# Kernel tuning notes

Measured on AMD Instinct MI355X. Metric: run time of the kernel, lower is better.

Reference implementation:

```python
import jax, jax.numpy as jnp
import numpy as np

NUM_HEADS = 8
WINDOW = 7      # window_size -> K = 49 neighbors
DILATION = 1


def setup_inputs() -> dict:
    key = jax.random.key(0)
    k1, k2, k3 = jax.random.split(key, 3)
    shape = (4, 256, 48, 48)  # [B, C, H, W], C = num_heads * d_head
    return {
        "q": jax.random.normal(k1, shape, jnp.float32),
        "k": jax.random.normal(k2, shape, jnp.float32),
        "v": jax.random.normal(k3, shape, jnp.float32),
    }


def _neighbors(x, window, dilation):
    # x: [B, h, d, H, W] -> [B, h, K, d, H, W] via pad-and-slice shifts
    B, h, d, H, W = x.shape
    r = window // 2
    p = r * dilation
    xp = jnp.pad(x, ((0, 0), (0, 0), (0, 0), (p, p), (p, p)))
    offs = [(i - r) * dilation for i in range(window)]
    sl = [xp[:, :, :, p + dy:p + dy + H, p + dx:p + dx + W]
          for dy in offs for dx in offs]
    return jnp.stack(sl, axis=2)


def _valid_mask(H, W, window, dilation):
    # [K, H, W] boolean: True where the shifted neighbor is in-bounds
    r = window // 2
    offs = np.array([(i - r) * dilation for i in range(window)])
    hy = np.arange(H)[None, :] + offs[:, None]  # [window, H]
    wx = np.arange(W)[None, :] + offs[:, None]  # [window, W]
    vh = (hy >= 0) & (hy < H)
    vw = (wx >= 0) & (wx < W)
    mask = vh[:, None, :, None] & vw[None, :, None, :]  # [window, window, H, W]
    return jnp.asarray(mask.reshape(window * window, H, W))


def reference(q, k, v):
    B, C, H, W = q.shape
    h = NUM_HEADS
    d = C // h
    qh = q.reshape(B, h, d, H, W)
    kh = k.reshape(B, h, d, H, W)
    vh = v.reshape(B, h, d, H, W)
    kn = _neighbors(kh, WINDOW, DILATION)  # [B,h,K,d,H,W]
    vn = _neighbors(vh, WINDOW, DILATION)
    mask = _valid_mask(H, W, WINDOW, DILATION)[None, None]  # [1,1,K,H,W]
    scores = jnp.einsum('bhdxy,bhkdxy->bhkxy', qh, kn) * (d ** -0.5)
    scores = jnp.where(mask, scores, jnp.finfo(scores.dtype).min)
    attn = jax.nn.softmax(scores, axis=2)
    out = jnp.einsum('bhkxy,bhkdxy->bhdxy', attn, vn)
    return out.reshape(B, C, H, W)  # merge_heads
```

## Files before the change

### kernel.cpp

```cpp
#include <hip/hip_runtime.h>


#define H_IMG 48
#define W_IMG 48
#define DHEAD 32
#define NH    8
#define RAD   3
#define TW    16
#define TH    6
#define NPART 4
#define CPL   8
#define HALO_W  (TW + 2*RAD)
#define HALO_H  (TH + 2*RAD)
#define HALO_PX (HALO_W * HALO_H)
#define CSTR    40
#define PLANE   (H_IMG * W_IMG)
#define NTHREADS (NPART * TW * TH)

typedef _Float16 half_t;
typedef half_t half2_t __attribute__((ext_vector_type(2)));

__device__ __forceinline__ float dppadd1(float x) {
  int y = __builtin_amdgcn_update_dpp(0, __float_as_int(x), 0xB1, 0xF, 0xF, true);
  return x + __int_as_float(y);
}
__device__ __forceinline__ float dppadd2(float x) {
  int y = __builtin_amdgcn_update_dpp(0, __float_as_int(x), 0x4E, 0xF, 0xF, true);
  return x + __int_as_float(y);
}

__global__ __launch_bounds__(NTHREADS, 4)
void natten_f32_kernel(const float* __restrict__ q,
                       const float* __restrict__ k,
                       const float* __restrict__ v,
                       float* __restrict__ out) {
  __shared__ __align__(16) unsigned short kl[(HALO_PX + 1) * CSTR];
  __shared__ __align__(16) unsigned short vl[(HALO_PX + 1) * CSTR];

  const int part = threadIdx.x;
  const int qx   = threadIdx.y;
  const int qy   = threadIdx.z;
  const int tid  = part + NPART * qx + NPART * TW * qy;
  const int x0   = blockIdx.x * TW;
  const int y0   = blockIdx.y * TH;
  const size_t cbase = (size_t)blockIdx.z * DHEAD * PLANE;

  for (int i = tid; i < HALO_PX * 2 * (DHEAD / 2); i += NTHREADS) {
    const int p    = i % HALO_PX;
    const int rest = i / HALO_PX;
    const int j    = rest & 15;
    const float* __restrict__ src = (rest & 16) ? v : k;
    unsigned short* dst           = (rest & 16) ? vl : kl;
    const int hy = p / HALO_W;
    const int hx = p - hy * HALO_W;
    const int gy = y0 - RAD + hy;
    const int gx = x0 - RAD + hx;
    union { half2_t h; unsigned int u; } pk;
    pk.u = 0;
    if ((unsigned)gy < (unsigned)H_IMG && (unsigned)gx < (unsigned)W_IMG) {
      const size_t g = cbase + (size_t)(2 * j) * PLANE + (size_t)gy * W_IMG + gx;
      pk.h.x = (half_t)src[g];
      pk.h.y = (half_t)src[g + PLANE];
    }
    *(unsigned int*)&dst[p * CSTR + 2 * j] = pk.u;
  }
  if (tid < CSTR) {
    kl[HALO_PX * CSTR + tid] = 0;
    vl[HALO_PX * CSTR + tid] = 0;
  }

  const int gqx = x0 + qx, gqy = y0 + qy;
  const float S = 0.17677669529663687f;
  const size_t qoff = cbase + (size_t)gqy * W_IMG + gqx;
  half2_t qp[4];
#pragma unroll
  for (int j = 0; j < 4; ++j) {
    qp[j].x = (half_t)(q[qoff + (size_t)(part * CPL + 2 * j) * PLANE] * S);
    qp[j].y = (half_t)(q[qoff + (size_t)(part * CPL + 2 * j + 1) * PLANE] * S);
  }

  unsigned colmask = 0;
#pragma unroll
  for (int rx = 0; rx < 7; ++rx) {
    const int gx = gqx + rx - RAD;
    if ((unsigned)gx < (unsigned)W_IMG) colmask |= (1u << rx);
  }

  __syncthreads();

  float den = 0.0f;
  float o[CPL];
#pragma unroll
  for (int j = 0; j < CPL; ++j) o[j] = 0.0f;

  for (int ry = 0; ry < 2 * RAD + 1; ++ry) {
    const int gy = gqy + ry - RAD;
    const unsigned mrow = ((unsigned)gy < (unsigned)H_IMG) ? colmask : 0u;
    const int base = ((qy + ry) * HALO_W + qx) * CSTR + part * CPL;
    const unsigned short* kb = &kl[base];
    const unsigned short* vb = &vl[base];
#pragma unroll
    for (int rx = 0; rx < 8; ++rx) {
      union { uint4 u; half2_t h[4]; } kw, vw;
      kw.u = *(const uint4*)(kb + rx * CSTR);
      vw.u = *(const uint4*)(vb + rx * CSTR);
      float acc = __builtin_amdgcn_fdot2(qp[0], kw.h[0], 0.0f, false);
      acc = __builtin_amdgcn_fdot2(qp[1], kw.h[1], acc, false);
      acc = __builtin_amdgcn_fdot2(qp[2], kw.h[2], acc, false);
      acc = __builtin_amdgcn_fdot2(qp[3], kw.h[3], acc, false);
      acc = dppadd1(acc);
      acc = dppadd2(acc);
      const float pe = __expf(acc);
      const float p = (mrow & (1u << rx)) ? pe : 0.0f;
      den += p;
      o[0] += p * (float)vw.h[0].x;  o[1] += p * (float)vw.h[0].y;
      o[2] += p * (float)vw.h[1].x;  o[3] += p * (float)vw.h[1].y;
      o[4] += p * (float)vw.h[2].x;  o[5] += p * (float)vw.h[2].y;
      o[6] += p * (float)vw.h[3].x;  o[7] += p * (float)vw.h[3].y;
    }
  }

  const float rden = 1.0f / den;
#pragma unroll
  for (int j = 0; j < CPL; ++j)
    out[qoff + (size_t)(part * CPL + j) * PLANE] = o[j] * rden;
}

extern "C" void kernel_launch(void* const* d_in, const int* in_sizes, int n_in,
                              void* d_out, int out_size, void* d_ws, size_t ws_size,
                              hipStream_t stream) {
  const float* q = (const float*)d_in[0];
  const float* k = (const float*)d_in[1];
  const float* v = (const float*)d_in[2];
  float* out = (float*)d_out;

  dim3 grid(W_IMG / TW, H_IMG / TH, 4 * NH);
  dim3 block(NPART, TW, TH);
  hipLaunchKernelGGL(natten_f32_kernel, grid, block, 0, stream, q, k, v, out);
}
```

Before: 110.1 us.

## Compute neighborhood QK and PV with MFMA over a 32-wide band per row

Replaces the per-thread fdot2 dot products with 16x16x32 f16 MFMA instructions. Each wave handles one query row of 16 pixels and computes scores against a 32-pixel band of keys per window row, masking out-of-window entries. The exponentiated probabilities go through a per-wave LDS buffer and are then multiplied by V with another MFMA. K and V are staged in new LDS layouts (V transposed to channel-major) so they fit the MFMA operands. The cost is computing scores for 32 band columns instead of the 7 window columns, plus the extra LDS round trip for the probabilities.

```diff
diff --git a/kernel.cpp b/kernel.cpp
--- a/kernel.cpp
+++ b/kernel.cpp
@@ -5,125 +5,147 @@
 #define W_IMG 48
 #define DHEAD 32
 #define NH    8
-#define RAD   3
+#define PLANE (H_IMG * W_IMG)
 #define TW    16
 #define TH    6
-#define NPART 4
-#define CPL   8
-#define HALO_W  (TW + 2*RAD)
-#define HALO_H  (TH + 2*RAD)
-#define HALO_PX (HALO_W * HALO_H)
-#define CSTR    40
-#define PLANE   (H_IMG * W_IMG)
-#define NTHREADS (NPART * TW * TH)
+#define KROWS 12
+#define KSTR  36
+#define VSTR  392
+#define PSTR  36
 
 typedef _Float16 half_t;
 typedef half_t half2_t __attribute__((ext_vector_type(2)));
+typedef half_t half8_t __attribute__((ext_vector_type(8)));
+typedef float  f32x4   __attribute__((ext_vector_type(4)));
 
-__device__ __forceinline__ float dppadd1(float x) {
-  int y = __builtin_amdgcn_update_dpp(0, __float_as_int(x), 0xB1, 0xF, 0xF, true);
-  return x + __int_as_float(y);
-}
-__device__ __forceinline__ float dppadd2(float x) {
-  int y = __builtin_amdgcn_update_dpp(0, __float_as_int(x), 0x4E, 0xF, 0xF, true);
-  return x + __int_as_float(y);
-}
+__global__ __launch_bounds__(64 * TH, 2)
+void natten_mfma_kernel(const float* __restrict__ q,
+                        const float* __restrict__ k,
+                        const float* __restrict__ v,
+                        float* __restrict__ out) {
+  __shared__ __align__(16) unsigned short kl[KROWS * 32 * KSTR];
+  __shared__ __align__(16) unsigned short vl[DHEAD * VSTR];
+  __shared__ __align__(16) unsigned short Pbuf[TH * TW * PSTR];
 
-__global__ __launch_bounds__(NTHREADS, 4)
-void natten_f32_kernel(const float* __restrict__ q,
-                       const float* __restrict__ k,
-                       const float* __restrict__ v,
-                       float* __restrict__ out) {
-  __shared__ __align__(16) unsigned short kl[(HALO_PX + 1) * CSTR];
-  __shared__ __align__(16) unsigned short vl[(HALO_PX + 1) * CSTR];
-
-  const int part = threadIdx.x;
-  const int qx   = threadIdx.y;
-  const int qy   = threadIdx.z;
-  const int tid  = part + NPART * qx + NPART * TW * qy;
+  const int lane = threadIdx.x;
+  const int wy   = threadIdx.y;
+  const int tid  = wy * 64 + lane;
   const int x0   = blockIdx.x * TW;
   const int y0   = blockIdx.y * TH;
   const size_t cbase = (size_t)blockIdx.z * DHEAD * PLANE;
 
-  for (int i = tid; i < HALO_PX * 2 * (DHEAD / 2); i += NTHREADS) {
-    const int p    = i % HALO_PX;
-    const int rest = i / HALO_PX;
-    const int j    = rest & 15;
-    const float* __restrict__ src = (rest & 16) ? v : k;
-    unsigned short* dst           = (rest & 16) ? vl : kl;
-    const int hy = p / HALO_W;
-    const int hx = p - hy * HALO_W;
-    const int gy = y0 - RAD + hy;
-    const int gx = x0 - RAD + hx;
-    union { half2_t h; unsigned int u; } pk;
-    pk.u = 0;
+  for (int i = tid; i < 16 * KROWS * 32; i += 64 * TH) {
+    const int px = i & 31;
+    const int t  = i >> 5;
+    const int hr = t % KROWS;
+    const int c  = t / KROWS;
+    const int gy = y0 - 3 + hr, gx = x0 - 3 + px;
+    union { half2_t h; unsigned u; } pk; pk.u = 0;
     if ((unsigned)gy < (unsigned)H_IMG && (unsigned)gx < (unsigned)W_IMG) {
-      const size_t g = cbase + (size_t)(2 * j) * PLANE + (size_t)gy * W_IMG + gx;
-      pk.h.x = (half_t)src[g];
-      pk.h.y = (half_t)src[g + PLANE];
+      const float* kb = k + cbase + (size_t)(2 * c) * PLANE + gy * W_IMG + gx;
+      pk.h.x = (half_t)kb[0];
+      pk.h.y = (half_t)kb[PLANE];
     }
-    *(unsigned int*)&dst[p * CSTR + 2 * j] = pk.u;
+    *(unsigned*)&kl[(hr * 32 + px) * KSTR + 2 * c] = pk.u;
   }
-  if (tid < CSTR) {
-    kl[HALO_PX * CSTR + tid] = 0;
-    vl[HALO_PX * CSTR + tid] = 0;
+  for (int i = tid; i < DHEAD * KROWS * 16; i += 64 * TH) {
+    const int xp = i & 15;
+    const int t  = i >> 4;
+    const int hr = t % KROWS;
+    const int ch = t / KROWS;
+    const int gy = y0 - 3 + hr;
+    const int gx0 = x0 - 3 + 2 * xp;
+    union { half2_t h; unsigned u; } pv; pv.u = 0;
+    if ((unsigned)gy < (unsigned)H_IMG) {
+      const float* vb = v + cbase + (size_t)ch * PLANE + gy * W_IMG;
+      if ((unsigned)gx0 < (unsigned)W_IMG)       pv.h.x = (half_t)vb[gx0];
+      if ((unsigned)(gx0 + 1) < (unsigned)W_IMG) pv.h.y = (half_t)vb[gx0 + 1];
+    }
+    *(unsigned*)&vl[ch * VSTR + hr * 32 + 2 * xp] = pv.u;
   }
 
-  const int gqx = x0 + qx, gqy = y0 + qy;
+  const int qi = lane & 15;
+  const int Q  = lane >> 4;
+  const int gqy = y0 + wy;
   const float S = 0.17677669529663687f;
-  const size_t qoff = cbase + (size_t)gqy * W_IMG + gqx;
-  half2_t qp[4];
+  union { half8_t h; uint4 u; } qf;
+  {
+    const float* qb = q + cbase + (size_t)gqy * W_IMG + x0 + qi;
 #pragma unroll
-  for (int j = 0; j < 4; ++j) {
-    qp[j].x = (half_t)(q[qoff + (size_t)(part * CPL + 2 * j) * PLANE] * S);
-    qp[j].y = (half_t)(q[qoff + (size_t)(part * CPL + 2 * j + 1) * PLANE] * S);
+    for (int j = 0; j < 8; ++j)
+      qf.h[j] = (half_t)(qb[(size_t)(Q * 8 + j) * PLANE] * S);
   }
 
-  unsigned colmask = 0;
-#pragma unroll
-  for (int rx = 0; rx < 7; ++rx) {
-    const int gx = gqx + rx - RAD;
-    if ((unsigned)gx < (unsigned)W_IMG) colmask |= (1u << rx);
-  }
+  const int xq = x0 + qi;
+  const int lft = (xq < 3) ? xq : 3;
+  const int rgt = (47 - xq < 3) ? (47 - xq) : 3;
+  const unsigned pm = ((1u << (lft + rgt + 1)) - 1u) << (qi + 3 - lft);
 
   __syncthreads();
 
-  float den = 0.0f;
-  float o[CPL];
+  unsigned short* Pb = &Pbuf[wy * TW * PSTR];
+  f32x4 o0 = {0.f, 0.f, 0.f, 0.f};
+  f32x4 o1 = {0.f, 0.f, 0.f, 0.f};
+  float den_l = 0.f;
+
+  for (int d = 0; d < 7; ++d) {
+    const int hr = wy + d;
+    const int gy = gqy + d - 3;
+    const unsigned pmr = ((unsigned)gy < (unsigned)H_IMG) ? pm : 0u;
+
+    const unsigned short* krow = &kl[hr * 32 * KSTR];
+    union { uint4 u; half8_t h; } A0, A1;
+    {
+      const unsigned short* p0 = &krow[qi * KSTR + Q * 8];
+      const unsigned short* p1 = &krow[(qi + 16) * KSTR + Q * 8];
+      uint2 a = *(const uint2*)p0, b = *(const uint2*)(p0 + 4);
+      uint2 c = *(const uint2*)p1, e = *(const uint2*)(p1 + 4);
+      A0.u = make_uint4(a.x, a.y, b.x, b.y);
+      A1.u = make_uint4(c.x, c.y, e.x, e.y);
+    }
+    f32x4 zero = {0.f, 0.f, 0.f, 0.f};
+    f32x4 s0 = __builtin_amdgcn_mfma_f32_16x16x32_f16(A0.h, qf.h, zero, 0, 0, 0);
+    f32x4 s1 = __builtin_amdgcn_mfma_f32_16x16x32_f16(A1.h, qf.h, zero, 0, 0, 0);
+
+    union { half_t h[4]; uint2 u; } w0, w1;
 #pragma unroll
-  for (int j = 0; j < CPL; ++j) o[j] = 0.0f;
+    for (int r = 0; r < 4; ++r) {
+      const int p0i = 4 * Q + r;
+      const float e0 = (pmr >> p0i) & 1 ? __expf(s0[r]) : 0.f;
+      const float e1 = (pmr >> (p0i + 16)) & 1 ? __expf(s1[r]) : 0.f;
+      den_l += e0 + e1;
+      w0.h[r] = (half_t)e0;
+      w1.h[r] = (half_t)e1;
+    }
+    *(uint2*)&Pb[qi * PSTR + 4 * Q]      = w0.u;
+    *(uint2*)&Pb[qi * PSTR + 16 + 4 * Q] = w1.u;
+    __builtin_amdgcn_wave_barrier();
+    union { uint4 u; half8_t h; } Pf;
+    {
+      const unsigned short* pр = &Pb[qi * PSTR + 8 * Q];
+      uint2 a = *(const uint2*)pр, b = *(const uint2*)(pр + 4);
+      Pf.u = make_uint4(a.x, a.y, b.x, b.y);
+    }
+    __builtin_amdgcn_wave_barrier();
 
-  for (int ry = 0; ry < 2 * RAD + 1; ++ry) {
-    const int gy = gqy + ry - RAD;
-    const unsigned mrow = ((unsigned)gy < (unsigned)H_IMG) ? colmask : 0u;
-    const int base = ((qy + ry) * HALO_W + qx) * CSTR + part * CPL;
-    const unsigned short* kb = &kl[base];
-    const unsigned short* vb = &vl[base];
-#pragma unroll
-    for (int rx = 0; rx < 8; ++rx) {
-      union { uint4 u; half2_t h[4]; } kw, vw;
-      kw.u = *(const uint4*)(kb + rx * CSTR);
-      vw.u = *(const uint4*)(vb + rx * CSTR);
-      float acc = __builtin_amdgcn_fdot2(qp[0], kw.h[0], 0.0f, false);
-      acc = __builtin_amdgcn_fdot2(qp[1], kw.h[1], acc, false);
-      acc = __builtin_amdgcn_fdot2(qp[2], kw.h[2], acc, false);
-      acc = __builtin_amdgcn_fdot2(qp[3], kw.h[3], acc, false);
-      acc = dppadd1(acc);
-      acc = dppadd2(acc);
-      const float pe = __expf(acc);
-      const float p = (mrow & (1u << rx)) ? pe : 0.0f;
-      den += p;
-      o[0] += p * (float)vw.h[0].x;  o[1] += p * (float)vw.h[0].y;
-      o[2] += p * (float)vw.h[1].x;  o[3] += p * (float)vw.h[1].y;
-      o[4] += p * (float)vw.h[2].x;  o[5] += p * (float)vw.h[2].y;
-      o[6] += p * (float)vw.h[3].x;  o[7] += p * (float)vw.h[3].y;
-    }
+    union { uint4 u; half8_t h; } V0, V1;
+    V0.u = *(const uint4*)&vl[qi * VSTR + hr * 32 + 8 * Q];
+    V1.u = *(const uint4*)&vl[(qi + 16) * VSTR + hr * 32 + 8 * Q];
+
+    o0 = __builtin_amdgcn_mfma_f32_16x16x32_f16(V0.h, Pf.h, o0, 0, 0, 0);
+    o1 = __builtin_amdgcn_mfma_f32_16x16x32_f16(V1.h, Pf.h, o1, 0, 0, 0);
   }
 
-  const float rden = 1.0f / den;
+  den_l += __shfl_xor(den_l, 16, 64);
+  den_l += __shfl_xor(den_l, 32, 64);
+  const float rden = 1.0f / den_l;
+
+  float* ob = out + cbase + (size_t)gqy * W_IMG + x0 + qi;
 #pragma unroll
-  for (int j = 0; j < CPL; ++j)
-    out[qoff + (size_t)(part * CPL + j) * PLANE] = o[j] * rden;
+  for (int r = 0; r < 4; ++r) {
+    ob[(size_t)(4 * Q + r) * PLANE]      = o0[r] * rden;
+    ob[(size_t)(16 + 4 * Q + r) * PLANE] = o1[r] * rden;
+  }
 }
 
 extern "C" void kernel_launch(void* const* d_in, const int* in_sizes, int n_in,
@@ -135,6 +157,6 @@
   float* out = (float*)d_out;
 
   dim3 grid(W_IMG / TW, H_IMG / TH, 4 * NH);
-  dim3 block(NPART, TW, TH);
-  hipLaunchKernelGGL(natten_f32_kernel, grid, block, 0, stream, q, k, v, out);
+  dim3 block(64, TH);
+  hipLaunchKernelGGL(natten_mfma_kernel, grid, block, 0, stream, q, k, v, out);
 }
```

Result: slower. 124.3 us (+12.9%).

## Use two lanes per query, exp2 softmax, and packed fp16 PV accumulation

Applied to the files above, without the earlier changes.

Each query is now split across 2 lanes of 16 channels instead of 4 lanes of 8, and the tile grows to 16x8. This halves the DPP reductions and lets the halo be shared by more queries. Scores are pre-scaled by log2(e) and go through a native exp2, with masked neighbors set to a large negative value instead of being selected after exp. The output accumulates in packed half2 FMA instead of fp32. That cuts VALU work but risks precision loss, since unnormalized fp16 sums could lose accuracy or overflow.

```diff
diff --git a/kernel.cpp b/kernel.cpp
--- a/kernel.cpp
+++ b/kernel.cpp
@@ -7,15 +7,13 @@
 #define NH    8
 #define RAD   3
 #define TW    16
-#define TH    6
-#define NPART 4
-#define CPL   8
+#define TH    8
 #define HALO_W  (TW + 2*RAD)
 #define HALO_H  (TH + 2*RAD)
 #define HALO_PX (HALO_W * HALO_H)
-#define CSTR    40
+#define CSTR    36
 #define PLANE   (H_IMG * W_IMG)
-#define NTHREADS (NPART * TW * TH)
+#define NTHREADS 256
 
 typedef _Float16 half_t;
 typedef half_t half2_t __attribute__((ext_vector_type(2)));
@@ -24,12 +22,8 @@
   int y = __builtin_amdgcn_update_dpp(0, __float_as_int(x), 0xB1, 0xF, 0xF, true);
   return x + __int_as_float(y);
 }
-__device__ __forceinline__ float dppadd2(float x) {
-  int y = __builtin_amdgcn_update_dpp(0, __float_as_int(x), 0x4E, 0xF, 0xF, true);
-  return x + __int_as_float(y);
-}
 
-__global__ __launch_bounds__(NTHREADS, 4)
+__global__ __launch_bounds__(NTHREADS, 3)
 void natten_f32_kernel(const float* __restrict__ q,
                        const float* __restrict__ k,
                        const float* __restrict__ v,
@@ -40,29 +34,28 @@
   const int part = threadIdx.x;
   const int qx   = threadIdx.y;
   const int qy   = threadIdx.z;
-  const int tid  = part + NPART * qx + NPART * TW * qy;
+  const int tid  = part + 2 * qx + 32 * qy;
   const int x0   = blockIdx.x * TW;
   const int y0   = blockIdx.y * TH;
   const size_t cbase = (size_t)blockIdx.z * DHEAD * PLANE;
 
-  for (int i = tid; i < HALO_PX * 2 * (DHEAD / 2); i += NTHREADS) {
-    const int p    = i % HALO_PX;
+  for (int i = tid; i < HALO_PX * 32; i += NTHREADS) {
+    const int px   = i % HALO_PX;
     const int rest = i / HALO_PX;
     const int j    = rest & 15;
     const float* __restrict__ src = (rest & 16) ? v : k;
     unsigned short* dst           = (rest & 16) ? vl : kl;
-    const int hy = p / HALO_W;
-    const int hx = p - hy * HALO_W;
+    const int hy = px / HALO_W;
+    const int hx = px - hy * HALO_W;
     const int gy = y0 - RAD + hy;
     const int gx = x0 - RAD + hx;
-    union { half2_t h; unsigned int u; } pk;
-    pk.u = 0;
+    union { half2_t h; unsigned u; } pk; pk.u = 0;
     if ((unsigned)gy < (unsigned)H_IMG && (unsigned)gx < (unsigned)W_IMG) {
       const size_t g = cbase + (size_t)(2 * j) * PLANE + (size_t)gy * W_IMG + gx;
       pk.h.x = (half_t)src[g];
       pk.h.y = (half_t)src[g + PLANE];
     }
-    *(unsigned int*)&dst[p * CSTR + 2 * j] = pk.u;
+    *(unsigned*)&dst[px * CSTR + 2 * j] = pk.u;
   }
   if (tid < CSTR) {
     kl[HALO_PX * CSTR + tid] = 0;
@@ -70,13 +63,13 @@
   }
 
   const int gqx = x0 + qx, gqy = y0 + qy;
-  const float S = 0.17677669529663687f;
+  const float Sl = 0.17677669529663687f * 1.4426950408889634f;
   const size_t qoff = cbase + (size_t)gqy * W_IMG + gqx;
-  half2_t qp[4];
+  half2_t qp[8];
 #pragma unroll
-  for (int j = 0; j < 4; ++j) {
-    qp[j].x = (half_t)(q[qoff + (size_t)(part * CPL + 2 * j) * PLANE] * S);
-    qp[j].y = (half_t)(q[qoff + (size_t)(part * CPL + 2 * j + 1) * PLANE] * S);
+  for (int j = 0; j < 8; ++j) {
+    qp[j].x = (half_t)(q[qoff + (size_t)(part * 16 + 2 * j) * PLANE] * Sl);
+    qp[j].y = (half_t)(q[qoff + (size_t)(part * 16 + 2 * j + 1) * PLANE] * Sl);
   }
 
   unsigned colmask = 0;
@@ -89,41 +82,54 @@
   __syncthreads();
 
   float den = 0.0f;
-  float o[CPL];
+  half2_t o[8];
 #pragma unroll
-  for (int j = 0; j < CPL; ++j) o[j] = 0.0f;
+  for (int j = 0; j < 8; ++j) o[j] = (half2_t)(half_t)0;
 
   for (int ry = 0; ry < 2 * RAD + 1; ++ry) {
     const int gy = gqy + ry - RAD;
     const unsigned mrow = ((unsigned)gy < (unsigned)H_IMG) ? colmask : 0u;
-    const int base = ((qy + ry) * HALO_W + qx) * CSTR + part * CPL;
+    const int base = ((qy + ry) * HALO_W + qx) * CSTR + part * 16;
     const unsigned short* kb = &kl[base];
     const unsigned short* vb = &vl[base];
 #pragma unroll
     for (int rx = 0; rx < 8; ++rx) {
-      union { uint4 u; half2_t h[4]; } kw, vw;
-      kw.u = *(const uint4*)(kb + rx * CSTR);
-      vw.u = *(const uint4*)(vb + rx * CSTR);
-      float acc = __builtin_amdgcn_fdot2(qp[0], kw.h[0], 0.0f, false);
-      acc = __builtin_amdgcn_fdot2(qp[1], kw.h[1], acc, false);
-      acc = __builtin_amdgcn_fdot2(qp[2], kw.h[2], acc, false);
-      acc = __builtin_amdgcn_fdot2(qp[3], kw.h[3], acc, false);
+      union { uint2 u[4]; half2_t h[8]; } kw, vw;
+      kw.u[0] = *(const uint2*)(kb + rx * CSTR);
+      kw.u[1] = *(const uint2*)(kb + rx * CSTR + 4);
+      kw.u[2] = *(const uint2*)(kb + rx * CSTR + 8);
+      kw.u[3] = *(const uint2*)(kb + rx * CSTR + 12);
+      float a0 = __builtin_amdgcn_fdot2(qp[0], kw.h[0], 0.0f, false);
+      a0 = __builtin_amdgcn_fdot2(qp[1], kw.h[1], a0, false);
+      a0 = __builtin_amdgcn_fdot2(qp[2], kw.h[2], a0, false);
+      a0 = __builtin_amdgcn_fdot2(qp[3], kw.h[3], a0, false);
+      float a1 = __builtin_amdgcn_fdot2(qp[4], kw.h[4], 0.0f, false);
+      a1 = __builtin_amdgcn_fdot2(qp[5], kw.h[5], a1, false);
+      a1 = __builtin_amdgcn_fdot2(qp[6], kw.h[6], a1, false);
+      a1 = __builtin_amdgcn_fdot2(qp[7], kw.h[7], a1, false);
+      float acc = a0 + a1;
       acc = dppadd1(acc);
-      acc = dppadd2(acc);
-      const float pe = __expf(acc);
-      const float p = (mrow & (1u << rx)) ? pe : 0.0f;
+      acc = (mrow & (1u << rx)) ? acc : -100000.0f;
+      const float p = __builtin_amdgcn_exp2f(acc);
       den += p;
-      o[0] += p * (float)vw.h[0].x;  o[1] += p * (float)vw.h[0].y;
-      o[2] += p * (float)vw.h[1].x;  o[3] += p * (float)vw.h[1].y;
-      o[4] += p * (float)vw.h[2].x;  o[5] += p * (float)vw.h[2].y;
-      o[6] += p * (float)vw.h[3].x;  o[7] += p * (float)vw.h[3].y;
+      const half_t ph = (half_t)p;
+      const half2_t p2 = {ph, ph};
+      vw.u[0] = *(const uint2*)(vb + rx * CSTR);
+      vw.u[1] = *(const uint2*)(vb + rx * CSTR + 4);
+      vw.u[2] = *(const uint2*)(vb + rx * CSTR + 8);
+      vw.u[3] = *(const uint2*)(vb + rx * CSTR + 12);
+#pragma unroll
+      for (int j = 0; j < 8; ++j)
+        o[j] += p2 * vw.h[j];
     }
   }
 
   const float rden = 1.0f / den;
 #pragma unroll
-  for (int j = 0; j < CPL; ++j)
-    out[qoff + (size_t)(part * CPL + j) * PLANE] = o[j] * rden;
+  for (int j = 0; j < 8; ++j) {
+    out[qoff + (size_t)(part * 16 + 2 * j) * PLANE]     = (float)o[j].x * rden;
+    out[qoff + (size_t)(part * 16 + 2 * j + 1) * PLANE] = (float)o[j].y * rden;
+  }
 }
 
 extern "C" void kernel_launch(void* const* d_in, const int* in_sizes, int n_in,
@@ -135,6 +141,6 @@
   float* out = (float*)d_out;
 
   dim3 grid(W_IMG / TW, H_IMG / TH, 4 * NH);
-  dim3 block(NPART, TW, TH);
+  dim3 block(2, TW, TH);
   hipLaunchKernelGGL(natten_f32_kernel, grid, block, 0, stream, q, k, v, out);
 }
```

Result: no change. 111.4 us (+1.2%).
